# Kernel optimization log

Hardware: AMD Instinct MI355X
Metric: run time of the kernel (lower is better)

Reference implementation:

```python
import jax, jax.numpy as jnp
import numpy as np

ALPHA = 0.5
INV_COEFF = 25.0
STD_COEFF = 25.0
COV_COEFF = 1.0
NUM_MATCHES = 50
EPS = 1e-5
GAMMA = 1.0


def _cdist(a, b):
    # (B,M,C),(B,N,C) -> (B,M,N) euclidean, matmul-based like torch.cdist
    a2 = jnp.sum(a * a, axis=-1, keepdims=True)            # (B,M,1)
    b2 = jnp.sum(b * b, axis=-1, keepdims=True)            # (B,N,1)
    d2 = a2 + jnp.swapaxes(b2, -1, -2) - 2.0 * jnp.einsum('bmc,bnc->bmn', a, b)
    return jnp.sqrt(jnp.maximum(d2, 0.0))


def _nn_match(input_maps, candidate_maps, distances, num_matches):
    # topk(k=1, largest=False) == min/argmin over last dim
    nn_dists = jnp.min(distances, axis=-1)                 # (B,M)
    nn_indices = jnp.argmin(distances, axis=-1)            # (B,M)
    # k smallest nn_dists, ascending order
    _, best_input_idx = jax.lax.top_k(-nn_dists, num_matches)   # (B,k)
    best_cand_idx = jnp.take_along_axis(nn_indices, best_input_idx, axis=1)
    filt_in = jnp.take_along_axis(input_maps, best_input_idx[:, :, None], axis=1)
    filt_cand = jnp.take_along_axis(candidate_maps, best_cand_idx[:, :, None], axis=1)
    return filt_in, filt_cand


def _off_diag_sq_sum(c):
    return jnp.sum(c * c) - jnp.sum(jnp.diag(c) ** 2)


def _std_term(x_flat):
    # unbiased variance over sample dim (torch var default)
    std = jnp.sqrt(jnp.var(x_flat, axis=0, ddof=1) + EPS)
    return jnp.mean(jax.nn.relu(GAMMA - std)) / 2.0


def _cov_term(x_flat):
    n, c = x_flat.shape
    xc = x_flat - jnp.mean(x_flat, axis=0)
    cov = xc.T @ xc / (n - 1)
    return _off_diag_sq_sum(cov) / c


def _vicreg_global(x, y):
    inv = jnp.mean((x - y) ** 2)
    std = _std_term(x) + _std_term(y)
    cov = _cov_term(x) + _cov_term(y)
    return INV_COEFF * inv + STD_COEFF * std + COV_COEFF * cov


def _vicregl_maps(x, y):
    # x, y: (B, k, C)
    inv = jnp.mean((x - y) ** 2)
    xf = x.reshape(-1, x.shape[-1])
    yf = y.reshape(-1, y.shape[-1])
    std = _std_term(xf) + _std_term(yf)
    cov = _cov_term(xf) + _cov_term(yf)
    return INV_COEFF * inv, STD_COEFF * std, COV_COEFF * cov


def _local_loss(spatial_1, spatial_2):
    B, C, H, W = spatial_1.shape
    maps_1 = spatial_1.reshape(B, C, H * W).transpose(0, 2, 1)   # (B,HW,C)
    maps_2 = spatial_2.reshape(B, C, H * W).transpose(0, 2, 1)
    d12 = _cdist(maps_1, maps_2)
    m1f, m1n = _nn_match(maps_1, maps_2, d12, NUM_MATCHES)
    d21 = _cdist(maps_2, maps_1)
    m2f, m2n = _nn_match(maps_2, maps_1, d21, NUM_MATCHES)
    inv1, var1, cov1 = _vicregl_maps(m1f, m1n)
    inv2, var2, cov2 = _vicregl_maps(m2f, m2n)
    return (inv1 + inv2) / 2 + (var1 + var2) / 2 + (cov1 + cov2) / 2


def setup_inputs() -> dict:
    key = jax.random.key(0)
    k1, k2, k3, k4 = jax.random.split(key, 4)
    B, C, H, W = 64, 768, 24, 24
    return {
        'spatial_1': jax.random.normal(k1, (B, C, H, W), dtype=jnp.float32),
        'pooled_1': jax.random.normal(k2, (B, C), dtype=jnp.float32),
        'spatial_2': jax.random.normal(k3, (B, C, H, W), dtype=jnp.float32),
        'pooled_2': jax.random.normal(k4, (B, C), dtype=jnp.float32),
    }


def reference(spatial_1, pooled_1, spatial_2, pooled_2):
    global_loss = _vicreg_global(pooled_1, pooled_2)
    local_loss = _local_loss(spatial_1, spatial_2)
    return ALPHA * global_loss + (1.0 - ALPHA) * local_loss
```

## Files before the change

### kernel.cpp

```cpp
#include <hip/hip_runtime.h>
#include <stdint.h>

typedef unsigned long long ull;
typedef unsigned int uint;
typedef unsigned short ushort;

typedef __attribute__((ext_vector_type(8))) short short8;
typedef __attribute__((ext_vector_type(4))) float floatx4;

#define B   64
#define C   768
#define HW  576
#define K   50
#define NLOC (B*K)

#define OFF_SLOTS   0
#define OFF_COLSUM  256
#define OFF_NN1     18688
#define OFF_NN2     313600
#define OFF_SELP    608512
#define OFF_SELQ    634112
#define OFF_NORM    659712
#define OFF_XT      954624
#define OFF_MP      OFF_XT
#define OFF_XGT     114200832
#define OFF_M       133861632

#define SLOT_INVG 0
#define SLOT_STD  1
#define SLOT_COV  7
#define SLOT_INV1 13
#define SLOT_INV2 14

__device__ __forceinline__ ull umin64(ull a, ull b) { return a < b ? a : b; }

__device__ __forceinline__ float bf2f_lo(uint u) { return __uint_as_float(u << 16); }
__device__ __forceinline__ float bf2f_hi(uint u) { return __uint_as_float(u & 0xffff0000u); }
__device__ __forceinline__ float bf2f(ushort u) { return __uint_as_float(((uint)u) << 16); }

__device__ __forceinline__ ushort f2bf(float f) {
    uint u = __float_as_uint(f);
    uint r = (u + 0x7fffu + ((u >> 16) & 1u)) >> 16;
    return (ushort)r;
}

__device__ __forceinline__ float blk_reduce_sum(float v, float* s4) {
    for (int off = 32; off > 0; off >>= 1) v += __shfl_down(v, off, 64);
    int lane = threadIdx.x & 63, w = threadIdx.x >> 6;
    if (lane == 0) s4[w] = v;
    __syncthreads();
    float r = 0.f;
    if (threadIdx.x == 0) r = s4[0] + s4[1] + s4[2] + s4[3];
    return r;
}

__global__ __launch_bounds__(256) void convert_kernel(const float* __restrict__ x1,
                                                      const float* __restrict__ x2,
                                                      ushort* __restrict__ xT,
                                                      float* __restrict__ normp) {
    int z = blockIdx.y;
    int which = z >> 6, b = z & 63;
    int half = blockIdx.x & 1;
    int pt = blockIdx.x >> 1;
    int p0 = pt * 64, c0 = half * 384;
    const float* X = (which ? x2 : x1) + ((size_t)b * C + c0) * HW + p0;

    __shared__ ushort tile[64][392];
    __shared__ float nlds[64][4];

    int t = threadIdx.x;
    int pq = t & 15, cq = t >> 4;
    int w = t >> 6;

    float ss[4] = {0.f, 0.f, 0.f, 0.f};

#pragma unroll
    for (int pass = 0; pass < 6; ++pass) {
        floatx4 v[4];
#pragma unroll
        for (int i = 0; i < 4; ++i)
            v[i] = *(const floatx4*)(X + (size_t)(pass * 64 + 4 * cq + i) * HW + 4 * pq);
#pragma unroll
        for (int j = 0; j < 4; ++j) {
            ushort u0 = f2bf(v[0][j]), u1 = f2bf(v[1][j]);
            ushort u2 = f2bf(v[2][j]), u3 = f2bf(v[3][j]);
            ushort4 uu; uu.x = u0; uu.y = u1; uu.z = u2; uu.w = u3;
            *(ushort4*)&tile[4 * pq + j][pass * 64 + 4 * cq] = uu;
            float r0 = bf2f(u0), r1 = bf2f(u1), r2 = bf2f(u2), r3 = bf2f(u3);
            ss[j] = fmaf(r0, r0, ss[j]); ss[j] = fmaf(r1, r1, ss[j]);
            ss[j] = fmaf(r2, r2, ss[j]); ss[j] = fmaf(r3, r3, ss[j]);
        }
    }
#pragma unroll
    for (int j = 0; j < 4; ++j) {
        ss[j] += __shfl_xor(ss[j], 16, 64);
        ss[j] += __shfl_xor(ss[j], 32, 64);
    }
    if ((t & 63) < 16) {
#pragma unroll
        for (int j = 0; j < 4; ++j) nlds[4 * pq + j][w] = ss[j];
    }
    __syncthreads();

    ushort* dst = xT + (((size_t)which * B + b) * HW + p0) * C + c0;
    const char* tb = (const char*)tile;
#pragma unroll
    for (int step = 0; step < 12; ++step) {
        int ib = (step * 256 + t) * 16;
        int p = ib / 768, cb = ib % 768;
        short8 vv = *(const short8*)(tb + (size_t)p * 784 + cb);
        *(short8*)(dst + (size_t)p * C + (cb >> 1)) = vv;
    }
    if (t < 64) {
        float nv = nlds[t][0] + nlds[t][1] + nlds[t][2] + nlds[t][3];
        normp[((size_t)half * 128 + which * 64 + b) * HW + p0 + t] = nv;
    }
}

template<int NK>
__device__ __forceinline__ void gemm_pp(const ushort* (&gA)[2][2], const ushort* (&gB)[2][2],
                                        char* (&dA)[2][2], char* (&dB)[2][2],
                                        const char* As, const char* Bs,
                                        const int (&offA)[4], const int (&offB)[4],
                                        floatx4 (&acc)[4][4]) {
    auto issue = [&](int s, int k0) {
#pragma unroll
        for (int n = 0; n < 2; ++n) {
            __builtin_amdgcn_global_load_lds(
                (const __attribute__((address_space(1))) void*)(gA[s][n] + k0),
                (__attribute__((address_space(3))) void*)dA[s][n], 16, 0, 0);
            __builtin_amdgcn_global_load_lds(
                (const __attribute__((address_space(1))) void*)(gB[s][n] + k0),
                (__attribute__((address_space(3))) void*)dB[s][n], 16, 0, 0);
        }
    };
    auto compute = [&](int s) {
        short8 a[4], bb[4];
#pragma unroll
        for (int i = 0; i < 4; ++i) a[i] = *(const short8*)(As + s * 8192 + offA[i]);
#pragma unroll
        for (int j = 0; j < 4; ++j) bb[j] = *(const short8*)(Bs + s * 8192 + offB[j]);
#pragma unroll
        for (int i = 0; i < 4; ++i)
#pragma unroll
            for (int j = 0; j < 4; ++j)
                acc[i][j] = __builtin_amdgcn_mfma_f32_16x16x32_bf16(a[i], bb[j], acc[i][j], 0, 0, 0);
    };

    issue(0, 0);
    issue(1, 0);
    for (int k = 0; k < NK; ++k) {
        asm volatile("s_waitcnt vmcnt(4)" ::: "memory");
        __builtin_amdgcn_s_barrier();
        __builtin_amdgcn_sched_barrier(0);
        compute(0);
        __builtin_amdgcn_sched_barrier(0);
        __builtin_amdgcn_s_barrier();
        if (k + 1 < NK) {
            issue(0, (k + 1) * 64);
            asm volatile("s_waitcnt vmcnt(4)" ::: "memory");
        } else {
            asm volatile("s_waitcnt vmcnt(0)" ::: "memory");
        }
        __builtin_amdgcn_s_barrier();
        __builtin_amdgcn_sched_barrier(0);
        compute(1);
        __builtin_amdgcn_sched_barrier(0);
        __builtin_amdgcn_s_barrier();
        if (k + 1 < NK) issue(1, (k + 1) * 64);
    }
}

__global__ __launch_bounds__(256) void cdist_mfma(const ushort* __restrict__ xT,
                                                  const float* __restrict__ normp,
                                                  ull* __restrict__ nn1,
                                                  ull* __restrict__ nn2) {
    int id = blockIdx.x;
    int xcd = id & 7, slot = id >> 3;
    int b = xcd + 8 * (slot / 25);
    int t = slot % 25;
    int qt = t % 5, pt = t / 5;

    const ushort* X1 = xT + (size_t)b * HW * C;
    const ushort* X2 = xT + (size_t)(B + b) * HW * C;

    __shared__ ull pool[4224];
    char* As = (char*)pool;
    char* Bs = As + 16384;

    int tid = threadIdx.x;
    int w = tid >> 6, l = tid & 63;
    int quad = l >> 4, col = l & 15;
    int lrow = l >> 2, pos = l & 3;

    const ushort* gA[2][2]; const ushort* gB[2][2];
    char* dA[2][2]; char* dB[2][2];
#pragma unroll
    for (int n = 0; n < 2; ++n) {
        int sm = w * 32 + n * 16 + lrow;
        int cdat = pos ^ ((sm >> 1) & 3);
        int p = pt * 128 + sm; if (p >= HW) p = HW - 1;
        int q = qt * 128 + sm; if (q >= HW) q = HW - 1;
#pragma unroll
        for (int s = 0; s < 2; ++s) {
            gA[s][n] = X1 + (size_t)p * C + s * 32 + cdat * 8;
            gB[s][n] = X2 + (size_t)q * C + s * 32 + cdat * 8;
            dA[s][n] = As + s * 8192 + w * 2048 + n * 1024;
            dB[s][n] = Bs + s * 8192 + w * 2048 + n * 1024;
        }
    }

    int offA[4], offB[4];
#pragma unroll
    for (int i = 0; i < 4; ++i) {
        int m_loc = (w >> 1) * 64 + i * 16 + col;
        offA[i] = m_loc * 64 + ((quad ^ ((m_loc >> 1) & 3)) * 16);
        int n_loc = (w & 1) * 64 + i * 16 + col;
        offB[i] = n_loc * 64 + ((quad ^ ((n_loc >> 1) & 3)) * 16);
    }

    floatx4 zero = {0.f, 0.f, 0.f, 0.f};
    floatx4 acc[4][4];
#pragma unroll
    for (int i = 0; i < 4; ++i)
#pragma unroll
        for (int j = 0; j < 4; ++j) acc[i][j] = zero;

    gemm_pp<12>(gA, gB, dA, dB, As, Bs, offA, offB, acc);

    const float* n1a = normp + (size_t)b * HW;
    const float* n1b = normp + (size_t)(128 + b) * HW;
    const float* n2a = normp + (size_t)(64 + b) * HW;
    const float* n2b = normp + (size_t)(192 + b) * HW;
    float n1v[4][4]; bool vp[4][4];
    float n2v[4];    bool vq[4];
#pragma unroll
    for (int i = 0; i < 4; ++i)
#pragma unroll
        for (int r = 0; r < 4; ++r) {
            int p = pt * 128 + (w >> 1) * 64 + i * 16 + quad * 4 + r;
            vp[i][r] = (p < HW);
            int pc = p < HW ? p : (HW - 1);
            n1v[i][r] = n1a[pc] + n1b[pc];
        }
#pragma unroll
    for (int j = 0; j < 4; ++j) {
        int q = qt * 128 + (w & 1) * 64 + j * 16 + col;
        vq[j] = (q < HW);
        int qc = q < HW ? q : (HW - 1);
        n2v[j] = n2a[qc] + n2b[qc];
    }

    __syncthreads();
    typedef ull row33[33];
    row33* red = (row33*)pool;

#pragma unroll
    for (int i = 0; i < 4; ++i)
#pragma unroll
        for (int r = 0; r < 4; ++r) {
            int p_loc = (w >> 1) * 64 + i * 16 + quad * 4 + r;
            ull best = ~0ull;
#pragma unroll
            for (int j = 0; j < 4; ++j) {
                if (!vq[j]) continue;
                float d2 = fmaxf(n1v[i][r] + n2v[j] - 2.0f * acc[i][j][r], 0.0f);
                unsigned q_glob = qt * 128 + (w & 1) * 64 + j * 16 + col;
                best = umin64(best, ((ull)__float_as_uint(d2) << 32) | q_glob);
            }
            red[p_loc][(w & 1) * 16 + col] = best;
        }
    __syncthreads();
    if (tid < 128) {
        int p_glob = pt * 128 + tid;
        ull m = ~0ull;
#pragma unroll
        for (int x = 0; x < 32; ++x) m = umin64(m, red[tid][x]);
        if (p_glob < HW) atomicMin(&nn1[(size_t)b * HW + p_glob], m);
    }
    __syncthreads();
#pragma unroll
    for (int j = 0; j < 4; ++j) {
        int q_loc = (w & 1) * 64 + j * 16 + col;
        ull best = ~0ull;
#pragma unroll
        for (int i = 0; i < 4; ++i)
#pragma unroll
            for (int r = 0; r < 4; ++r) {
                if (!vp[i][r]) continue;
                float d2 = fmaxf(n1v[i][r] + n2v[j] - 2.0f * acc[i][j][r], 0.0f);
                unsigned p_glob = pt * 128 + (w >> 1) * 64 + i * 16 + quad * 4 + r;
                best = umin64(best, ((ull)__float_as_uint(d2) << 32) | p_glob);
            }
        red[q_loc][(w >> 1) * 4 + quad] = best;
    }
    __syncthreads();
    if (tid < 128) {
        int q_glob = qt * 128 + tid;
        ull m = ~0ull;
#pragma unroll
        for (int x = 0; x < 8; ++x) m = umin64(m, red[tid][x]);
        if (q_glob < HW) atomicMin(&nn2[(size_t)b * HW + q_glob], m);
    }
}

__global__ __launch_bounds__(64) void select_topk_wave(const ull* __restrict__ nn1,
                                                       const ull* __restrict__ nn2,
                                                       int* __restrict__ sel_p,
                                                       int* __restrict__ sel_q) {
    int b = blockIdx.x, dir = blockIdx.y;
    const ull* nn = dir ? nn2 : nn1;
    int lane = threadIdx.x;
    ull key[9]; uint qv[9];
#pragma unroll
    for (int r = 0; r < 9; ++r) {
        int p = r * 64 + lane;
        ull e = nn[(size_t)b * HW + p];
        key[r] = (e & 0xFFFFFFFF00000000ull) | (unsigned)p;
        qv[r] = (uint)(e & 0xFFFFFFFFu);
    }
    int* sp = sel_p + (dir * B + b) * K;
    int* sq = sel_q + (dir * B + b) * K;
    for (int it = 0; it < K; ++it) {
        ull m = key[0];
#pragma unroll
        for (int r = 1; r < 9; ++r) m = umin64(m, key[r]);
#pragma unroll
        for (int off = 32; off > 0; off >>= 1) m = umin64(m, __shfl_xor(m, off, 64));
#pragma unroll
        for (int r = 0; r < 9; ++r) {
            if (key[r] == m) {
                sp[it] = (int)(uint)(m & 0xFFFFFFFFu);
                sq[it] = (int)qv[r];
                key[r] = ~0ull;
            }
        }
    }
}

__global__ __launch_bounds__(256) void gather_jmajor(const ushort* __restrict__ xT,
                                                     const int* __restrict__ sel_p,
                                                     const int* __restrict__ sel_q,
                                                     ushort* __restrict__ XgT) {
    int j = blockIdx.x, s = blockIdx.y;
    int dir = s >> 1;
    int whichsrc = (s == 1 || s == 2) ? 1 : 0;
    const int* sel = (s & 1) ? sel_q : sel_p;
    __shared__ int sidx[64];
    __shared__ uint buf[64][33];
    int tid = threadIdx.x;
    if (tid < 64) sidx[tid] = sel[(dir * B + tid) * K + j];
    __syncthreads();
    int rb = tid >> 2, u = tid & 3;
    const ushort* srow = xT + (((size_t)whichsrc * B + rb) * HW + sidx[rb]) * C;
    int wv = tid >> 6, lb = tid & 63;
    ushort* obase = XgT + (size_t)s * C * NLOC + (size_t)j * 64 + lb;
    for (int ch = 0; ch < 12; ++ch) {
        __syncthreads();
        uint4 v0 = *(const uint4*)(srow + ch * 64 + u * 8);
        uint4 v1 = *(const uint4*)(srow + ch * 64 + (u + 4) * 8);
        buf[rb][u * 4 + 0] = v0.x; buf[rb][u * 4 + 1] = v0.y;
        buf[rb][u * 4 + 2] = v0.z; buf[rb][u * 4 + 3] = v0.w;
        buf[rb][(u + 4) * 4 + 0] = v1.x; buf[rb][(u + 4) * 4 + 1] = v1.y;
        buf[rb][(u + 4) * 4 + 2] = v1.z; buf[rb][(u + 4) * 4 + 3] = v1.w;
        __syncthreads();
#pragma unroll
        for (int st = 0; st < 16; ++st) {
            int cl = wv + st * 4;
            uint uv = buf[lb][cl >> 1];
            ushort val = (cl & 1) ? (ushort)(uv >> 16) : (ushort)(uv & 0xffffu);
            obase[(size_t)(ch * 64 + cl) * NLOC] = val;
        }
    }
}

__global__ __launch_bounds__(256) void ata_mfma(const ushort* __restrict__ XgT,
                                                float* __restrict__ Mp) {
    int bx = blockIdx.x;
    int mat = blockIdx.y, split = blockIdx.z;
    int rt = bx / 6, ct = bx % 6;
    const ushort* X = XgT + (size_t)mat * C * NLOC;

    __shared__ ull pool[4096];
    char* As = (char*)pool;
    char* Bs = As + 16384;

    int tid = threadIdx.x;
    int w = tid >> 6, l = tid & 63;
    int quad = l >> 4, col = l & 15;
    int lrow = l >> 2, pos = l & 3;

    const ushort* gA[2][2]; const ushort* gB[2][2];
    char* dA[2][2]; char* dB[2][2];
#pragma unroll
    for (int n = 0; n < 2; ++n) {
        int sm = w * 32 + n * 16 + lrow;
        int cdat = pos ^ ((sm >> 1) & 3);
#pragma unroll
        for (int s = 0; s < 2; ++s) {
            gA[s][n] = X + (size_t)(rt * 128 + sm) * NLOC + split * 640 + s * 32 + cdat * 8;
            gB[s][n] = X + (size_t)(ct * 128 + sm) * NLOC + split * 640 + s * 32 + cdat * 8;
            dA[s][n] = As + s * 8192 + w * 2048 + n * 1024;
            dB[s][n] = Bs + s * 8192 + w * 2048 + n * 1024;
        }
    }

    int offA[4], offB[4];
#pragma unroll
    for (int i = 0; i < 4; ++i) {
        int m_loc = (w >> 1) * 64 + i * 16 + col;
        offA[i] = m_loc * 64 + ((quad ^ ((m_loc >> 1) & 3)) * 16);
        int n_loc = (w & 1) * 64 + i * 16 + col;
        offB[i] = n_loc * 64 + ((quad ^ ((n_loc >> 1) & 3)) * 16);
    }

    floatx4 zero = {0.f, 0.f, 0.f, 0.f};
    floatx4 acc[4][4];
#pragma unroll
    for (int i = 0; i < 4; ++i)
#pragma unroll
        for (int j = 0; j < 4; ++j) acc[i][j] = zero;

    gemm_pp<10>(gA, gB, dA, dB, As, Bs, offA, offB, acc);

    float* Mo = Mp + (size_t)(mat * 5 + split) * C * C;
#pragma unroll
    for (int i = 0; i < 4; ++i)
#pragma unroll
        for (int j = 0; j < 4; ++j)
#pragma unroll
            for (int r = 0; r < 4; ++r) {
                int row = rt * 128 + (w >> 1) * 64 + i * 16 + quad * 4 + r;
                int cc  = ct * 128 + (w & 1) * 64 + j * 16 + col;
                Mo[(size_t)row * C + cc] = acc[i][j][r];
            }
}

__global__ __launch_bounds__(256) void reduce_mp(const float* __restrict__ Mp,
                                                 float* __restrict__ M) {
    int mat = blockIdx.y;
    int i = blockIdx.x * 256 + threadIdx.x;
    float4 r = {0.f, 0.f, 0.f, 0.f};
#pragma unroll
    for (int s = 0; s < 5; ++s) {
        const float4* a = (const float4*)(Mp + (size_t)(mat * 5 + s) * C * C);
        float4 v = a[i];
        r.x += v.x; r.y += v.y; r.z += v.z; r.w += v.w;
    }
    ((float4*)(M + (size_t)mat * C * C))[i] = r;
}

__global__ __launch_bounds__(256) void ata_pooled(const float* __restrict__ p1,
                                                  const float* __restrict__ p2,
                                                  float* __restrict__ M) {
    int mat = 4 + blockIdx.z;
    const float* X = (mat == 4) ? p1 : p2;
    int n = B;
    float* Mo = M + (size_t)mat * C * C;
    int ct = blockIdx.x, rt = blockIdx.y;

    __shared__ float As[16][64];
    __shared__ float Bs[16][64];
    int tid = threadIdx.x;
    int tx = tid & 15, ty = tid >> 4;
    int lr = tid >> 4, lc = (tid & 15) * 4;

    float acc[4][4] = {};
    for (int k0 = 0; k0 < n; k0 += 16) {
        float4 av = *(const float4*)&X[(size_t)(k0 + lr) * C + rt * 64 + lc];
        float4 bv = *(const float4*)&X[(size_t)(k0 + lr) * C + ct * 64 + lc];
        __syncthreads();
        *(float4*)&As[lr][lc] = av;
        *(float4*)&Bs[lr][lc] = bv;
        __syncthreads();
#pragma unroll
        for (int kk = 0; kk < 16; ++kk) {
            float4 af = *(const float4*)&As[kk][ty * 4];
            float4 bf = *(const float4*)&Bs[kk][tx * 4];
            float a[4] = {af.x, af.y, af.z, af.w};
            float bb[4] = {bf.x, bf.y, bf.z, bf.w};
#pragma unroll
            for (int i = 0; i < 4; ++i)
#pragma unroll
                for (int j = 0; j < 4; ++j)
                    acc[i][j] = fmaf(a[i], bb[j], acc[i][j]);
        }
    }
#pragma unroll
    for (int i = 0; i < 4; ++i) {
        float4 o = {acc[i][0], acc[i][1], acc[i][2], acc[i][3]};
        *(float4*)&Mo[(size_t)(rt * 64 + ty * 4 + i) * C + ct * 64 + tx * 4] = o;
    }
}

__global__ __launch_bounds__(256) void colsum4_kernel(const ushort* __restrict__ XgT,
                                                      float* __restrict__ colsum) {
    int mat = blockIdx.y, cb = blockIdx.x * 4;
    int r = threadIdx.x >> 6, lane = threadIdx.x & 63;
    const ushort* row = XgT + ((size_t)mat * C + cb + r) * NLOC;
    float s = 0.f;
    for (int i = lane; i < NLOC; i += 64) s += bf2f(row[i]);
    for (int off = 32; off > 0; off >>= 1) s += __shfl_down(s, off, 64);
    if (lane == 0) colsum[mat * C + cb + r] = s;
}

__global__ __launch_bounds__(256) void colsum_pooled(const float* __restrict__ p1,
                                                     const float* __restrict__ p2,
                                                     float* __restrict__ colsum) {
    int mat = 4 + blockIdx.y;
    const float* X = (mat == 4) ? p1 : p2;
    int c = blockIdx.x * 256 + threadIdx.x;
    float s = 0.f;
    for (int r = 0; r < B; ++r) s += X[(size_t)r * C + c];
    colsum[mat * C + c] = s;
}

__global__ __launch_bounds__(256) void std_kernel(const float* __restrict__ M,
                                                  const float* __restrict__ colsum,
                                                  float* __restrict__ slots) {
    int mat = blockIdx.y;
    float n = (mat < 4) ? (float)NLOC : (float)B;
    int c = blockIdx.x * 256 + threadIdx.x;
    float r = 0.f;
    if (c < C) {
        float mcc = M[(size_t)mat * C * C + (size_t)c * C + c];
        float cs = colsum[mat * C + c];
        float var = (mcc - cs * cs / n) / (n - 1.0f);
        float sd = sqrtf(var + 1e-5f);
        float g = 1.0f - sd;
        r = g > 0.f ? g : 0.f;
    }
    __shared__ float s4[4];
    float t = blk_reduce_sum(r, s4);
    if (threadIdx.x == 0) atomicAdd(&slots[SLOT_STD + mat], t);
}

__global__ __launch_bounds__(256) void cov_kernel(const float* __restrict__ M,
                                                  const float* __restrict__ colsum,
                                                  float* __restrict__ slots) {
    int mat = blockIdx.y;
    float n = (mat < 4) ? (float)NLOC : (float)B;
    float invn1 = 1.0f / (n - 1.0f);
    const float* Mm = M + (size_t)mat * C * C;
    __shared__ float cs_s[C];
    for (int c = threadIdx.x; c < C; c += 256) cs_s[c] = colsum[mat * C + c];
    __syncthreads();
    float s = 0.f;
    int r0 = blockIdx.x * 16;
    for (int r = 0; r < 16; ++r) {
        int row = r0 + r;
        float csr = cs_s[row] / n;
        const float* Mr = Mm + (size_t)row * C;
        for (int c = threadIdx.x; c < C; c += 256) {
            float cv = (Mr[c] - csr * cs_s[c]) * invn1;
            if (c != row) s = fmaf(cv, cv, s);
        }
    }
    __shared__ float s4[4];
    float t = blk_reduce_sum(s, s4);
    if (threadIdx.x == 0) atomicAdd(&slots[SLOT_COV + mat], t);
}

__global__ __launch_bounds__(256) void inv_global_kernel(const float* __restrict__ p1,
                                                         const float* __restrict__ p2,
                                                         float* __restrict__ slots) {
    int idx = blockIdx.x * 256 + threadIdx.x;
    int stride = gridDim.x * 256;
    float s = 0.f;
    for (int i = idx; i < B * C; i += stride) {
        float d = p1[i] - p2[i];
        s = fmaf(d, d, s);
    }
    __shared__ float s4[4];
    float t = blk_reduce_sum(s, s4);
    if (threadIdx.x == 0) atomicAdd(&slots[SLOT_INVG], t);
}

__global__ __launch_bounds__(256) void inv_local2(const ushort* __restrict__ XgT,
                                                  float* __restrict__ slots) {
    int pair = blockIdx.y;
    const uint* A4 = (const uint*)(XgT + (size_t)(2 * pair) * C * NLOC);
    const uint* B4 = (const uint*)(XgT + (size_t)(2 * pair + 1) * C * NLOC);
    int idx = blockIdx.x * 256 + threadIdx.x;
    int stride = gridDim.x * 256;
    int n = C * NLOC / 2;
    float s = 0.f;
    for (int i = idx; i < n; i += stride) {
        uint ua = A4[i], ub = B4[i];
        float d0 = bf2f_lo(ua) - bf2f_lo(ub);
        float d1 = bf2f_hi(ua) - bf2f_hi(ub);
        s = fmaf(d0, d0, s);
        s = fmaf(d1, d1, s);
    }
    __shared__ float s4[4];
    float t = blk_reduce_sum(s, s4);
    if (threadIdx.x == 0) atomicAdd(&slots[(pair == 0) ? SLOT_INV1 : SLOT_INV2], t);
}

__global__ void final_kernel(const float* __restrict__ slots, float* __restrict__ out) {
    float std_t[6], cov_t[6];
    for (int m = 0; m < 6; ++m) {
        std_t[m] = slots[SLOT_STD + m] / (float)C * 0.5f;
        cov_t[m] = slots[SLOT_COV + m] / (float)C;
    }
    float inv_g = slots[SLOT_INVG] / (float)(B * C);
    float global_loss = 25.0f * inv_g + 25.0f * (std_t[4] + std_t[5]) + (cov_t[4] + cov_t[5]);
    float inv1 = 25.0f * slots[SLOT_INV1] / (float)(NLOC * C);
    float inv2 = 25.0f * slots[SLOT_INV2] / (float)(NLOC * C);
    float var1 = 25.0f * (std_t[0] + std_t[1]);
    float var2 = 25.0f * (std_t[2] + std_t[3]);
    float cov1 = cov_t[0] + cov_t[1];
    float cov2 = cov_t[2] + cov_t[3];
    float local_loss = (inv1 + inv2) * 0.5f + (var1 + var2) * 0.5f + (cov1 + cov2) * 0.5f;
    out[0] = 0.5f * global_loss + 0.5f * local_loss;
}

extern "C" void kernel_launch(void* const* d_in, const int* in_sizes, int n_in,
                              void* d_out, int out_size, void* d_ws, size_t ws_size,
                              hipStream_t stream) {
    const float* spatial_1 = (const float*)d_in[0];
    const float* pooled_1  = (const float*)d_in[1];
    const float* spatial_2 = (const float*)d_in[2];
    const float* pooled_2  = (const float*)d_in[3];
    float* out = (float*)d_out;

    char* ws = (char*)d_ws;
    float*  slots  = (float*)(ws + OFF_SLOTS);
    float*  colsum = (float*)(ws + OFF_COLSUM);
    ull*    nn1    = (ull*)(ws + OFF_NN1);
    ull*    nn2    = (ull*)(ws + OFF_NN2);
    int*    sel_p  = (int*)(ws + OFF_SELP);
    int*    sel_q  = (int*)(ws + OFF_SELQ);
    ushort* xT     = (ushort*)(ws + OFF_XT);
    float*  Mp     = (float*)(ws + OFF_MP);
    ushort* XgT    = (ushort*)(ws + OFF_XGT);
    float*  M      = (float*)(ws + OFF_M);
    float*  normp  = (float*)(ws + OFF_M);

    hipMemsetAsync(ws, 0, OFF_NN1, stream);
    hipMemsetAsync(ws + OFF_NN1, 0xFF, OFF_SELP - OFF_NN1, stream);

    convert_kernel<<<dim3(18, 128), 256, 0, stream>>>(spatial_1, spatial_2, xT, normp);
    cdist_mfma<<<1600, 256, 0, stream>>>(xT, normp, nn1, nn2);
    select_topk_wave<<<dim3(B, 2), 64, 0, stream>>>(nn1, nn2, sel_p, sel_q);
    gather_jmajor<<<dim3(K, 4), 256, 0, stream>>>(xT, sel_p, sel_q, XgT);
    ata_mfma<<<dim3(36, 4, 5), 256, 0, stream>>>(XgT, Mp);
    ata_pooled<<<dim3(12, 12, 2), 256, 0, stream>>>(pooled_1, pooled_2, M);
    reduce_mp<<<dim3(576, 4), 256, 0, stream>>>(Mp, M);
    colsum4_kernel<<<dim3(192, 4), 256, 0, stream>>>(XgT, colsum);
    colsum_pooled<<<dim3(3, 2), 256, 0, stream>>>(pooled_1, pooled_2, colsum);
    std_kernel<<<dim3(3, 6), 256, 0, stream>>>(M, colsum, slots);
    cov_kernel<<<dim3(48, 6), 256, 0, stream>>>(M, colsum, slots);
    inv_global_kernel<<<dim3(96), 256, 0, stream>>>(pooled_1, pooled_2, slots);
    inv_local2<<<dim3(300, 2), 256, 0, stream>>>(XgT, slots);
    final_kernel<<<1, 1, 0, stream>>>(slots, out);
}
```

Before: 472.9 us.

## Use 4-stage LDS ring with one barrier per step; fold split-K reduction into std/cov

The shared GEMM loop moves from a two-buffer, four-barrier-per-iteration schedule to a four-slot ring with three loads in flight and a single barrier per 32-wide k step. This is meant to hide global-to-LDS latency and cut synchronisation in the cdist and A^T A kernels. LDS per block doubles to 64KB, which may lower occupancy. The separate reduce_mp kernel is also removed: std and cov now sum the five split-K partials directly, saving a full pass over the partial matrices and one launch.

```diff
diff --git a/kernel.cpp b/kernel.cpp
--- a/kernel.cpp
+++ b/kernel.cpp
@@ -20,7 +20,6 @@
 #define OFF_NN2     313600
 #define OFF_SELP    608512
 #define OFF_SELQ    634112
-#define OFF_NORM    659712
 #define OFF_XT      954624
 #define OFF_MP      OFF_XT
 #define OFF_XGT     114200832
@@ -117,57 +116,42 @@
     }
 }
 
-template<int NK>
-__device__ __forceinline__ void gemm_pp(const ushort* (&gA)[2][2], const ushort* (&gB)[2][2],
-                                        char* (&dA)[2][2], char* (&dB)[2][2],
-                                        const char* As, const char* Bs,
+template<int NG>
+__device__ __forceinline__ void gemm_pp(const ushort* const (&gA)[2], const ushort* const (&gB)[2],
+                                        char* pool, int w,
                                         const int (&offA)[4], const int (&offB)[4],
                                         floatx4 (&acc)[4][4]) {
-    auto issue = [&](int s, int k0) {
+    auto issue = [&](int h) {
+        char* buf = pool + (h & 3) * 16384;
 #pragma unroll
         for (int n = 0; n < 2; ++n) {
             __builtin_amdgcn_global_load_lds(
-                (const __attribute__((address_space(1))) void*)(gA[s][n] + k0),
-                (__attribute__((address_space(3))) void*)dA[s][n], 16, 0, 0);
+                (const __attribute__((address_space(1))) void*)(gA[n] + h * 32),
+                (__attribute__((address_space(3))) void*)(buf + w * 2048 + n * 1024), 16, 0, 0);
             __builtin_amdgcn_global_load_lds(
-                (const __attribute__((address_space(1))) void*)(gB[s][n] + k0),
-                (__attribute__((address_space(3))) void*)dB[s][n], 16, 0, 0);
+                (const __attribute__((address_space(1))) void*)(gB[n] + h * 32),
+                (__attribute__((address_space(3))) void*)(buf + 8192 + w * 2048 + n * 1024), 16, 0, 0);
         }
     };
-    auto compute = [&](int s) {
+    issue(0); issue(1); issue(2);
+    for (int h = 0; h < NG; ++h) {
+        if (h < NG - 2)      asm volatile("s_waitcnt vmcnt(8)" ::: "memory");
+        else if (h == NG - 2) asm volatile("s_waitcnt vmcnt(4)" ::: "memory");
+        else                  asm volatile("s_waitcnt vmcnt(0)" ::: "memory");
+        __builtin_amdgcn_s_barrier();
+        if (h + 3 < NG) issue(h + 3);
+        __builtin_amdgcn_sched_barrier(0);
+        const char* buf = pool + (h & 3) * 16384;
         short8 a[4], bb[4];
 #pragma unroll
-        for (int i = 0; i < 4; ++i) a[i] = *(const short8*)(As + s * 8192 + offA[i]);
-#pragma unroll
-        for (int j = 0; j < 4; ++j) bb[j] = *(const short8*)(Bs + s * 8192 + offB[j]);
+        for (int i = 0; i < 4; ++i) a[i] = *(const short8*)(buf + offA[i]);
+#pragma unroll
+        for (int j = 0; j < 4; ++j) bb[j] = *(const short8*)(buf + 8192 + offB[j]);
 #pragma unroll
         for (int i = 0; i < 4; ++i)
 #pragma unroll
             for (int j = 0; j < 4; ++j)
                 acc[i][j] = __builtin_amdgcn_mfma_f32_16x16x32_bf16(a[i], bb[j], acc[i][j], 0, 0, 0);
-    };
-
-    issue(0, 0);
-    issue(1, 0);
-    for (int k = 0; k < NK; ++k) {
-        asm volatile("s_waitcnt vmcnt(4)" ::: "memory");
-        __builtin_amdgcn_s_barrier();
-        __builtin_amdgcn_sched_barrier(0);
-        compute(0);
-        __builtin_amdgcn_sched_barrier(0);
-        __builtin_amdgcn_s_barrier();
-        if (k + 1 < NK) {
-            issue(0, (k + 1) * 64);
-            asm volatile("s_waitcnt vmcnt(4)" ::: "memory");
-        } else {
-            asm volatile("s_waitcnt vmcnt(0)" ::: "memory");
-        }
-        __builtin_amdgcn_s_barrier();
-        __builtin_amdgcn_sched_barrier(0);
-        compute(1);
-        __builtin_amdgcn_sched_barrier(0);
-        __builtin_amdgcn_s_barrier();
-        if (k + 1 < NK) issue(1, (k + 1) * 64);
     }
 }
 
@@ -184,30 +168,23 @@
     const ushort* X1 = xT + (size_t)b * HW * C;
     const ushort* X2 = xT + (size_t)(B + b) * HW * C;
 
-    __shared__ ull pool[4224];
-    char* As = (char*)pool;
-    char* Bs = As + 16384;
+    __shared__ ull pool[8192];
+    char* poolc = (char*)pool;
 
     int tid = threadIdx.x;
     int w = tid >> 6, l = tid & 63;
     int quad = l >> 4, col = l & 15;
     int lrow = l >> 2, pos = l & 3;
 
-    const ushort* gA[2][2]; const ushort* gB[2][2];
-    char* dA[2][2]; char* dB[2][2];
+    const ushort* gA[2]; const ushort* gB[2];
 #pragma unroll
     for (int n = 0; n < 2; ++n) {
         int sm = w * 32 + n * 16 + lrow;
         int cdat = pos ^ ((sm >> 1) & 3);
         int p = pt * 128 + sm; if (p >= HW) p = HW - 1;
         int q = qt * 128 + sm; if (q >= HW) q = HW - 1;
-#pragma unroll
-        for (int s = 0; s < 2; ++s) {
-            gA[s][n] = X1 + (size_t)p * C + s * 32 + cdat * 8;
-            gB[s][n] = X2 + (size_t)q * C + s * 32 + cdat * 8;
-            dA[s][n] = As + s * 8192 + w * 2048 + n * 1024;
-            dB[s][n] = Bs + s * 8192 + w * 2048 + n * 1024;
-        }
+        gA[n] = X1 + (size_t)p * C + cdat * 8;
+        gB[n] = X2 + (size_t)q * C + cdat * 8;
     }
 
     int offA[4], offB[4];
@@ -226,7 +203,7 @@
 #pragma unroll
         for (int j = 0; j < 4; ++j) acc[i][j] = zero;
 
-    gemm_pp<12>(gA, gB, dA, dB, As, Bs, offA, offB, acc);
+    gemm_pp<24>(gA, gB, poolc, w, offA, offB, acc);
 
     const float* n1a = normp + (size_t)b * HW;
     const float* n1b = normp + (size_t)(128 + b) * HW;
@@ -381,28 +358,21 @@
     int rt = bx / 6, ct = bx % 6;
     const ushort* X = XgT + (size_t)mat * C * NLOC;
 
-    __shared__ ull pool[4096];
-    char* As = (char*)pool;
-    char* Bs = As + 16384;
+    __shared__ ull pool[8192];
+    char* poolc = (char*)pool;
 
     int tid = threadIdx.x;
     int w = tid >> 6, l = tid & 63;
     int quad = l >> 4, col = l & 15;
     int lrow = l >> 2, pos = l & 3;
 
-    const ushort* gA[2][2]; const ushort* gB[2][2];
-    char* dA[2][2]; char* dB[2][2];
+    const ushort* gA[2]; const ushort* gB[2];
 #pragma unroll
     for (int n = 0; n < 2; ++n) {
         int sm = w * 32 + n * 16 + lrow;
         int cdat = pos ^ ((sm >> 1) & 3);
-#pragma unroll
-        for (int s = 0; s < 2; ++s) {
-            gA[s][n] = X + (size_t)(rt * 128 + sm) * NLOC + split * 640 + s * 32 + cdat * 8;
-            gB[s][n] = X + (size_t)(ct * 128 + sm) * NLOC + split * 640 + s * 32 + cdat * 8;
-            dA[s][n] = As + s * 8192 + w * 2048 + n * 1024;
-            dB[s][n] = Bs + s * 8192 + w * 2048 + n * 1024;
-        }
+        gA[n] = X + (size_t)(rt * 128 + sm) * NLOC + split * 640 + cdat * 8;
+        gB[n] = X + (size_t)(ct * 128 + sm) * NLOC + split * 640 + cdat * 8;
     }
 
     int offA[4], offB[4];
@@ -421,7 +391,7 @@
 #pragma unroll
         for (int j = 0; j < 4; ++j) acc[i][j] = zero;
 
-    gemm_pp<10>(gA, gB, dA, dB, As, Bs, offA, offB, acc);
+    gemm_pp<20>(gA, gB, poolc, w, offA, offB, acc);
 
     float* Mo = Mp + (size_t)(mat * 5 + split) * C * C;
 #pragma unroll
@@ -434,20 +404,6 @@
                 int cc  = ct * 128 + (w & 1) * 64 + j * 16 + col;
                 Mo[(size_t)row * C + cc] = acc[i][j][r];
             }
-}
-
-__global__ __launch_bounds__(256) void reduce_mp(const float* __restrict__ Mp,
-                                                 float* __restrict__ M) {
-    int mat = blockIdx.y;
-    int i = blockIdx.x * 256 + threadIdx.x;
-    float4 r = {0.f, 0.f, 0.f, 0.f};
-#pragma unroll
-    for (int s = 0; s < 5; ++s) {
-        const float4* a = (const float4*)(Mp + (size_t)(mat * 5 + s) * C * C);
-        float4 v = a[i];
-        r.x += v.x; r.y += v.y; r.z += v.z; r.w += v.w;
-    }
-    ((float4*)(M + (size_t)mat * C * C))[i] = r;
 }
 
 __global__ __launch_bounds__(256) void ata_pooled(const float* __restrict__ p1,
@@ -515,7 +471,8 @@
     colsum[mat * C + c] = s;
 }
 
-__global__ __launch_bounds__(256) void std_kernel(const float* __restrict__ M,
+__global__ __launch_bounds__(256) void std_kernel(const float* __restrict__ Mp,
+                                                  const float* __restrict__ M,
                                                   const float* __restrict__ colsum,
                                                   float* __restrict__ slots) {
     int mat = blockIdx.y;
@@ -523,7 +480,15 @@
     int c = blockIdx.x * 256 + threadIdx.x;
     float r = 0.f;
     if (c < C) {
-        float mcc = M[(size_t)mat * C * C + (size_t)c * C + c];
+        float mcc;
+        if (mat < 4) {
+            mcc = 0.f;
+#pragma unroll
+            for (int s = 0; s < 5; ++s)
+                mcc += Mp[(size_t)(mat * 5 + s) * C * C + (size_t)c * C + c];
+        } else {
+            mcc = M[(size_t)mat * C * C + (size_t)c * C + c];
+        }
         float cs = colsum[mat * C + c];
         float var = (mcc - cs * cs / n) / (n - 1.0f);
         float sd = sqrtf(var + 1e-5f);
@@ -535,13 +500,13 @@
     if (threadIdx.x == 0) atomicAdd(&slots[SLOT_STD + mat], t);
 }
 
-__global__ __launch_bounds__(256) void cov_kernel(const float* __restrict__ M,
+__global__ __launch_bounds__(256) void cov_kernel(const float* __restrict__ Mp,
+                                                  const float* __restrict__ M,
                                                   const float* __restrict__ colsum,
                                                   float* __restrict__ slots) {
     int mat = blockIdx.y;
     float n = (mat < 4) ? (float)NLOC : (float)B;
     float invn1 = 1.0f / (n - 1.0f);
-    const float* Mm = M + (size_t)mat * C * C;
     __shared__ float cs_s[C];
     for (int c = threadIdx.x; c < C; c += 256) cs_s[c] = colsum[mat * C + c];
     __syncthreads();
@@ -550,10 +515,24 @@
     for (int r = 0; r < 16; ++r) {
         int row = r0 + r;
         float csr = cs_s[row] / n;
-        const float* Mr = Mm + (size_t)row * C;
-        for (int c = threadIdx.x; c < C; c += 256) {
-            float cv = (Mr[c] - csr * cs_s[c]) * invn1;
-            if (c != row) s = fmaf(cv, cv, s);
+        if (mat < 4) {
+            const float* Mr0 = Mp + (size_t)(mat * 5 + 0) * C * C + (size_t)row * C;
+            const float* Mr1 = Mp + (size_t)(mat * 5 + 1) * C * C + (size_t)row * C;
+            const float* Mr2 = Mp + (size_t)(mat * 5 + 2) * C * C + (size_t)row * C;
+            const float* Mr3 = Mp + (size_t)(mat * 5 + 3) * C * C + (size_t)row * C;
+            const float* Mr4 = Mp + (size_t)(mat * 5 + 4) * C * C + (size_t)row * C;
+            for (int c = threadIdx.x; c < C; c += 256) {
+                float v = Mr0[c];
+                v += Mr1[c]; v += Mr2[c]; v += Mr3[c]; v += Mr4[c];
+                float cv = (v - csr * cs_s[c]) * invn1;
+                if (c != row) s = fmaf(cv, cv, s);
+            }
+        } else {
+            const float* Mr = M + (size_t)mat * C * C + (size_t)row * C;
+            for (int c = threadIdx.x; c < C; c += 256) {
+                float cv = (Mr[c] - csr * cs_s[c]) * invn1;
+                if (c != row) s = fmaf(cv, cv, s);
+            }
         }
     }
     __shared__ float s4[4];
@@ -646,11 +625,10 @@
     gather_jmajor<<<dim3(K, 4), 256, 0, stream>>>(xT, sel_p, sel_q, XgT);
     ata_mfma<<<dim3(36, 4, 5), 256, 0, stream>>>(XgT, Mp);
     ata_pooled<<<dim3(12, 12, 2), 256, 0, stream>>>(pooled_1, pooled_2, M);
-    reduce_mp<<<dim3(576, 4), 256, 0, stream>>>(Mp, M);
     colsum4_kernel<<<dim3(192, 4), 256, 0, stream>>>(XgT, colsum);
     colsum_pooled<<<dim3(3, 2), 256, 0, stream>>>(pooled_1, pooled_2, colsum);
-    std_kernel<<<dim3(3, 6), 256, 0, stream>>>(M, colsum, slots);
-    cov_kernel<<<dim3(48, 6), 256, 0, stream>>>(M, colsum, slots);
+    std_kernel<<<dim3(3, 6), 256, 0, stream>>>(Mp, M, colsum, slots);
+    cov_kernel<<<dim3(48, 6), 256, 0, stream>>>(Mp, M, colsum, slots);
     inv_global_kernel<<<dim3(96), 256, 0, stream>>>(pooled_1, pooled_2, slots);
     inv_local2<<<dim3(300, 2), 256, 0, stream>>>(XgT, slots);
     final_kernel<<<1, 1, 0, stream>>>(slots, out);
```

Measured after the change: 470.2 us. About the same (-0.6%).
